# Performance work log

Measured on AMD Instinct MI355X. Metric: run time of the kernel, lower is better.

The kernel has to match this reference:

```python
import jax, jax.numpy as jnp
import numpy as np

B, S, HIDDEN = 2, 2048, 2048
HEADS, GROUPS, KVC = 16, 4, 128
HPG = HEADS // GROUPS  # heads per group
LAYER_INDEX = 2
SOFTMAX_SCALE = KVC ** -0.5
ROPE_THETA = 10000.0


def _rope_tables(seq_len, dim, dtype=jnp.float32):
    inv_freq = 1.0 / (ROPE_THETA ** (jnp.arange(0, dim, 2, dtype=jnp.float32) / dim))
    t = jnp.arange(seq_len, dtype=jnp.float32)
    freqs = jnp.outer(t, inv_freq)  # [S, dim/2]
    return jnp.cos(freqs).astype(dtype), jnp.sin(freqs).astype(dtype)


def _apply_rope(x, cos, sin):
    # x: [b, s, h, d]; rotate-half (GPT-NeoX style)
    d2 = x.shape[-1] // 2
    x1, x2 = x[..., :d2], x[..., d2:]
    c = cos[None, :, None, :]
    s = sin[None, :, None, :]
    return jnp.concatenate([x1 * c - x2 * s, x2 * c + x1 * s], axis=-1)


def setup_inputs() -> dict:
    key = jax.random.key(0)
    k1, k2, k3, k4 = jax.random.split(key, 4)
    std = HIDDEN ** -0.5
    return {
        "x": jax.random.normal(k1, (B, S, HIDDEN), dtype=jnp.float32),
        "w_q": jax.random.normal(k2, (HIDDEN, HEADS * KVC), dtype=jnp.float32) * std,
        "w_kv": jax.random.normal(k3, (HIDDEN, 2 * GROUPS * KVC), dtype=jnp.float32) * std,
        "w_dense": jax.random.normal(k4, (HEADS * KVC, HIDDEN), dtype=jnp.float32) * std,
    }


def reference(x, w_q, w_kv, w_dense):
    b, s, _ = x.shape
    # QKV projections
    q = (x @ w_q).reshape(b, s, HEADS, KVC)                 # [b,s,H,d]
    kv = (x @ w_kv).reshape(b, s, 2, GROUPS, KVC)
    k, v = kv[:, :, 0], kv[:, :, 1]                          # [b,s,G,d]
    # Rotary embeddings on q and k
    cos, sin = _rope_tables(s, KVC, x.dtype)
    q = _apply_rope(q, cos, sin)
    k = _apply_rope(k, cos, sin)
    # GQA attention with per-layer scaling trick:
    # scores computed at scale/softmax of layer_index, cast fp32, rescaled back.
    qg = q.reshape(b, s, GROUPS, HPG, KVC)
    scores = jnp.einsum("bqghd,bkgd->bghqk", qg, k) * (SOFTMAX_SCALE / LAYER_INDEX)
    scores = scores.astype(jnp.float32) * LAYER_INDEX
    # causal mask
    causal = jnp.tril(jnp.ones((s, s), dtype=bool))
    mask_value = jnp.finfo(jnp.float32).min
    scores = jnp.where(causal[None, None, None, :, :], scores, mask_value)
    probs = jax.nn.softmax(scores, axis=-1).astype(x.dtype)  # dropout p=0 (eval)
    ctx = jnp.einsum("bghqk,bkgd->bqghd", probs, v).reshape(b, s, HEADS * KVC)
    return ctx @ w_dense
```

## Files before the change

kernel.cpp:

```cpp
#include <hip/hip_runtime.h>
#include <hip/hip_bf16.h>
#include <stdint.h>

typedef unsigned short u16;
typedef __bf16 bf16x8 __attribute__((ext_vector_type(8)));
typedef float f32x4 __attribute__((ext_vector_type(4)));

#define S_LEN 2048
#define BATCH 2
#define NHEADS 16
#define NGROUPS 4
#define DHEAD 128
#define QKV_W 3072

__device__ __forceinline__ float bf2f(u16 u) {
  union { uint32_t i; float f; } v; v.i = ((uint32_t)u) << 16; return v.f;
}
__device__ __forceinline__ u16 f2bf(float f) {
  union { float f; uint32_t i; } v; v.f = f;
  uint32_t r = v.i + 0x7FFF + ((v.i >> 16) & 1);
  return (u16)(r >> 16);
}
__device__ __forceinline__ void llds16(const void* g, void* l) {
  __builtin_amdgcn_global_load_lds(
      (const __attribute__((address_space(1))) uint32_t*)g,
      (__attribute__((address_space(3))) uint32_t*)l, 16, 0, 0);
}

__device__ __forceinline__ void store_out(u16* C, long i, float v) { C[i] = f2bf(v); }
__device__ __forceinline__ void store_out(float* C, long i, float v) { C[i] = v; }

__global__ void rope_tables_k(float* __restrict__ cosT, float* __restrict__ sinT) {
  int i = blockIdx.x * 256 + threadIdx.x;
  int s = i >> 6, j = i & 63;
  float inv = exp2f(-(float)j * 0.20762050593045983f);
  float ang = (float)s * inv;
  float sv, cv;
  sincosf(ang, &sv, &cv);
  cosT[i] = cv; sinT[i] = sv;
}

__global__ void cvt_f32_bf16(const float* __restrict__ in, u16* __restrict__ out) {
  long i = ((long)blockIdx.x * 256 + threadIdx.x) * 4;
  float4 v = *(const float4*)(in + i);
  ushort4 o;
  o.x = f2bf(v.x); o.y = f2bf(v.y); o.z = f2bf(v.z); o.w = f2bf(v.w);
  *(ushort4*)(out + i) = o;
}

__global__ void transpose_f32_bf16(const float* __restrict__ in, u16* __restrict__ out,
                                   int R, int C) {
  __shared__ u16 tile[32][33];
  int c0 = blockIdx.x * 32, r0 = blockIdx.y * 32;
  int tx = threadIdx.x, ty = threadIdx.y;
  for (int i = 0; i < 32; i += 8)
    tile[ty + i][tx] = f2bf(in[(long)(r0 + ty + i) * C + c0 + tx]);
  __syncthreads();
  for (int i = 0; i < 32; i += 8)
    out[(long)(c0 + ty + i) * R + r0 + tx] = tile[tx][ty + i];
}

#define GFENCE() asm volatile("" ::: "memory")
#define MIDBAR() do { GFENCE(); __builtin_amdgcn_s_barrier(); \
    asm volatile("s_waitcnt lgkmcnt(0)" ::: "memory"); } while (0)
#define ENDBAR() do { GFENCE(); __builtin_amdgcn_s_barrier(); GFENCE(); } while (0)

__device__ __forceinline__ bf16x8 frag_ld(const __bf16* h, int wrow, int kk, int quad) {
  int b = ((wrow & 15) << 6) | (quad << 4);
  b ^= ((wrow >> 3) & 1) << 5;
  int off = ((((wrow >> 4) << 1) | kk) << 10) | b;
  return *(const bf16x8*)((const char*)h + off);
}

__device__ __forceinline__ void stage_half(const u16* __restrict__ g, int K,
                                           __bf16* lhalf, int wv, int lane) {
  int bsrc = (lane << 4) ^ (((lane >> 5) & 1) << 5);
  int r = bsrc >> 6, c = (bsrc & 63) >> 1;
  int cb = (wv & 1) << 5;
  llds16(g + (long)((wv >> 1) * 16 + r) * K + cb + c,
         lhalf + wv * 512 + lane * 8);
  llds16(g + (long)((4 + (wv >> 1)) * 16 + r) * K + cb + c,
         lhalf + 4096 + wv * 512 + lane * 8);
}

template <typename OutT>
__global__ __launch_bounds__(512) void gemm_bt8(
    const u16* __restrict__ A, const u16* __restrict__ Bt, OutT* __restrict__ C,
    int M, int N, int K) {
  __shared__ __align__(16) __bf16 lds[2][2][16384];
  const int tid = threadIdx.x;
  const int wv = tid >> 6, lane = tid & 63;
  const int quad = lane >> 4, l16 = lane & 15;
  const int wr = wv >> 2, wc = wv & 3;

  const int nwg = gridDim.x * gridDim.y;
  const int orig = blockIdx.y * gridDim.x + blockIdx.x;
  const int swz = (orig & 7) * (nwg >> 3) + (orig >> 3);
  const int bx = swz % gridDim.x, by = swz / gridDim.x;
  const int bm = by * 256, bn = bx * 256;

  const u16* Abase = A + (long)bm * K;
  const u16* Bbase = Bt + (long)bn * K;
  const int NT = K >> 6;

  f32x4 acc[8][4] = {};

  stage_half(Abase, K, &lds[0][0][0], wv, lane);
  stage_half(Abase + (long)128 * K, K, &lds[0][0][8192], wv, lane);
  stage_half(Bbase, K, &lds[0][1][0], wv, lane);
  stage_half(Bbase + (long)128 * K, K, &lds[0][1][8192], wv, lane);
  stage_half(Abase + 64, K, &lds[1][0][0], wv, lane);
  stage_half(Abase + (long)128 * K + 64, K, &lds[1][0][8192], wv, lane);
  stage_half(Bbase + 64, K, &lds[1][1][0], wv, lane);
  stage_half(Bbase + (long)128 * K + 64, K, &lds[1][1][8192], wv, lane);
  asm volatile("s_waitcnt vmcnt(8)" ::: "memory");
  __builtin_amdgcn_s_barrier();
  GFENCE();

  for (int kt = 0; kt < NT; ++kt) {
    const int buf = kt & 1;
    const __bf16* Ah = &lds[buf][0][wr * 8192];
    const __bf16* Bh = &lds[buf][1][(wc >> 1) * 8192];
    const int brow0 = (wc & 1) << 6;
    const bool pre = (kt + 2 < NT);
    bf16x8 aF[4][2], bF[4][2];

#pragma unroll
    for (int m = 0; m < 4; ++m) {
      aF[m][0] = frag_ld(Ah, m * 16 + l16, 0, quad);
      aF[m][1] = frag_ld(Ah, m * 16 + l16, 1, quad);
    }
#pragma unroll
    for (int n = 0; n < 2; ++n) {
      bF[n][0] = frag_ld(Bh, brow0 + n * 16 + l16, 0, quad);
      bF[n][1] = frag_ld(Bh, brow0 + n * 16 + l16, 1, quad);
    }
    MIDBAR();
    __builtin_amdgcn_s_setprio(1);
#pragma unroll
    for (int m = 0; m < 4; ++m)
#pragma unroll
      for (int n = 0; n < 2; ++n) {
        acc[m][n] = __builtin_amdgcn_mfma_f32_16x16x32_bf16(aF[m][0], bF[n][0], acc[m][n], 0, 0, 0);
        acc[m][n] = __builtin_amdgcn_mfma_f32_16x16x32_bf16(aF[m][1], bF[n][1], acc[m][n], 0, 0, 0);
      }
    __builtin_amdgcn_s_setprio(0);
    ENDBAR();

#pragma unroll
    for (int n = 2; n < 4; ++n) {
      bF[n][0] = frag_ld(Bh, brow0 + n * 16 + l16, 0, quad);
      bF[n][1] = frag_ld(Bh, brow0 + n * 16 + l16, 1, quad);
    }
    MIDBAR();
    __builtin_amdgcn_s_setprio(1);
#pragma unroll
    for (int m = 0; m < 4; ++m)
#pragma unroll
      for (int n = 2; n < 4; ++n) {
        acc[m][n] = __builtin_amdgcn_mfma_f32_16x16x32_bf16(aF[m][0], bF[n][0], acc[m][n], 0, 0, 0);
        acc[m][n] = __builtin_amdgcn_mfma_f32_16x16x32_bf16(aF[m][1], bF[n][1], acc[m][n], 0, 0, 0);
      }
    __builtin_amdgcn_s_setprio(0);
    ENDBAR();

#pragma unroll
    for (int m = 0; m < 4; ++m) {
      aF[m][0] = frag_ld(Ah, 64 + m * 16 + l16, 0, quad);
      aF[m][1] = frag_ld(Ah, 64 + m * 16 + l16, 1, quad);
    }
    if (pre) {
      const u16* p = Bbase + (long)(kt + 2) * 64;
      stage_half(p, K, &lds[buf][1][0], wv, lane);
      stage_half(p + (long)128 * K, K, &lds[buf][1][8192], wv, lane);
    }
    MIDBAR();
    __builtin_amdgcn_s_setprio(1);
#pragma unroll
    for (int m = 0; m < 4; ++m)
#pragma unroll
      for (int n = 2; n < 4; ++n) {
        acc[4 + m][n] = __builtin_amdgcn_mfma_f32_16x16x32_bf16(aF[m][0], bF[n][0], acc[4 + m][n], 0, 0, 0);
        acc[4 + m][n] = __builtin_amdgcn_mfma_f32_16x16x32_bf16(aF[m][1], bF[n][1], acc[4 + m][n], 0, 0, 0);
      }
    __builtin_amdgcn_s_setprio(0);
    ENDBAR();

    if (pre) {
      const u16* p = Abase + (long)(kt + 2) * 64;
      stage_half(p, K, &lds[buf][0][0], wv, lane);
      stage_half(p + (long)128 * K, K, &lds[buf][0][8192], wv, lane);
    }
    MIDBAR();
    __builtin_amdgcn_s_setprio(1);
#pragma unroll
    for (int m = 0; m < 4; ++m)
#pragma unroll
      for (int n = 0; n < 2; ++n) {
        acc[4 + m][n] = __builtin_amdgcn_mfma_f32_16x16x32_bf16(aF[m][0], bF[n][0], acc[4 + m][n], 0, 0, 0);
        acc[4 + m][n] = __builtin_amdgcn_mfma_f32_16x16x32_bf16(aF[m][1], bF[n][1], acc[4 + m][n], 0, 0, 0);
      }
    __builtin_amdgcn_s_setprio(0);
    if (pre) { asm volatile("s_waitcnt vmcnt(8)" ::: "memory"); }
    else     { asm volatile("s_waitcnt vmcnt(0)" ::: "memory"); }
    ENDBAR();
  }

  const long colbase = (long)bn + wc * 64 + l16;
#pragma unroll
  for (int mt = 0; mt < 8; ++mt)
#pragma unroll
    for (int nt = 0; nt < 4; ++nt)
#pragma unroll
      for (int rr = 0; rr < 4; ++rr) {
        long row = bm + wr * 128 + mt * 16 + quad * 4 + rr;
        store_out(C, row * N + colbase + nt * 16, acc[mt][nt][rr]);
      }
}

__global__ __launch_bounds__(512) void gemm_bt8n(
    const u16* __restrict__ A, const u16* __restrict__ Bt, float* __restrict__ C,
    int M, int N, int K) {
  __shared__ __align__(16) __bf16 Abuf[2][16384];
  __shared__ __align__(16) __bf16 Bbuf[2][8192];
  const int tid = threadIdx.x;
  const int wv = tid >> 6, lane = tid & 63;
  const int quad = lane >> 4, l16 = lane & 15;
  const int wr = wv >> 2, wc = wv & 3;

  const int nwg = gridDim.x * gridDim.y;
  const int orig = blockIdx.y * gridDim.x + blockIdx.x;
  const int swz = (orig & 7) * (nwg >> 3) + (orig >> 3);
  const int bx = swz % gridDim.x, by = swz / gridDim.x;
  const int bm = by * 256, bn = bx * 128;

  const u16* Abase = A + (long)bm * K;
  const u16* Bbase = Bt + (long)bn * K;
  const int NT = K >> 6;

  f32x4 acc[8][2] = {};

  stage_half(Abase, K, &Abuf[0][0], wv, lane);
  stage_half(Abase + (long)128 * K, K, &Abuf[0][8192], wv, lane);
  stage_half(Bbase, K, &Bbuf[0][0], wv, lane);
  stage_half(Abase + 64, K, &Abuf[1][0], wv, lane);
  stage_half(Abase + (long)128 * K + 64, K, &Abuf[1][8192], wv, lane);
  stage_half(Bbase + 64, K, &Bbuf[1][0], wv, lane);
  asm volatile("s_waitcnt vmcnt(0)" ::: "memory");
  __builtin_amdgcn_s_barrier();
  GFENCE();

  for (int kt = 0; kt < NT; ++kt) {
    const int buf = kt & 1;
    const __bf16* Ah = &Abuf[buf][wr * 8192];
    const __bf16* Bh = &Bbuf[buf][0];
    bf16x8 aF[4][2], bF[2][2];

#pragma unroll
    for (int m = 0; m < 4; ++m) {
      aF[m][0] = frag_ld(Ah, m * 16 + l16, 0, quad);
      aF[m][1] = frag_ld(Ah, m * 16 + l16, 1, quad);
    }
#pragma unroll
    for (int n = 0; n < 2; ++n) {
      bF[n][0] = frag_ld(Bh, wc * 32 + n * 16 + l16, 0, quad);
      bF[n][1] = frag_ld(Bh, wc * 32 + n * 16 + l16, 1, quad);
    }
    if (kt >= 1 && kt + 1 < NT) {
      const u16* p = Abase + (long)(kt + 1) * 64;
      stage_half(p, K, &Abuf[(kt + 1) & 1][0], wv, lane);
      stage_half(p + (long)128 * K, K, &Abuf[(kt + 1) & 1][8192], wv, lane);
    }
    MIDBAR();
    __builtin_amdgcn_s_setprio(1);
#pragma unroll
    for (int m = 0; m < 4; ++m)
#pragma unroll
      for (int n = 0; n < 2; ++n) {
        acc[m][n] = __builtin_amdgcn_mfma_f32_16x16x32_bf16(aF[m][0], bF[n][0], acc[m][n], 0, 0, 0);
        acc[m][n] = __builtin_amdgcn_mfma_f32_16x16x32_bf16(aF[m][1], bF[n][1], acc[m][n], 0, 0, 0);
      }
    __builtin_amdgcn_s_setprio(0);
    ENDBAR();

#pragma unroll
    for (int m = 0; m < 4; ++m) {
      aF[m][0] = frag_ld(Ah, 64 + m * 16 + l16, 0, quad);
      aF[m][1] = frag_ld(Ah, 64 + m * 16 + l16, 1, quad);
    }
    if (kt + 2 < NT) {
      stage_half(Bbase + (long)(kt + 2) * 64, K, &Bbuf[buf][0], wv, lane);
    }
    MIDBAR();
    __builtin_amdgcn_s_setprio(1);
#pragma unroll
    for (int m = 0; m < 4; ++m)
#pragma unroll
      for (int n = 0; n < 2; ++n) {
        acc[4 + m][n] = __builtin_amdgcn_mfma_f32_16x16x32_bf16(aF[m][0], bF[n][0], acc[4 + m][n], 0, 0, 0);
        acc[4 + m][n] = __builtin_amdgcn_mfma_f32_16x16x32_bf16(aF[m][1], bF[n][1], acc[4 + m][n], 0, 0, 0);
      }
    __builtin_amdgcn_s_setprio(0);
    if (kt + 2 < NT) { asm volatile("s_waitcnt vmcnt(2)" ::: "memory"); }
    else             { asm volatile("s_waitcnt vmcnt(0)" ::: "memory"); }
    ENDBAR();
  }

  const long colbase = (long)bn + wc * 32 + l16;
#pragma unroll
  for (int mt = 0; mt < 8; ++mt)
#pragma unroll
    for (int nt = 0; nt < 2; ++nt)
#pragma unroll
      for (int rr = 0; rr < 4; ++rr) {
        long row = bm + wr * 128 + mt * 16 + quad * 4 + rr;
        C[row * N + colbase + nt * 16] = acc[mt][nt][rr];
      }
}

__global__ void rope_k_k(const u16* __restrict__ qkv, u16* __restrict__ Kb,
                         const float* __restrict__ cosT, const float* __restrict__ sinT) {
  long i = (long)blockIdx.x * 256 + threadIdx.x;
  int j = i & 63;
  long rest = i >> 6;
  int g = rest & 3;
  long bs = rest >> 2;
  int s = bs & (S_LEN - 1);
  int b = (int)(bs >> 11);
  long src = bs * QKV_W + 2048 + g * 128 + j;
  float x1 = bf2f(qkv[src]), x2 = bf2f(qkv[src + 64]);
  float c = cosT[s * 64 + j], sn = sinT[s * 64 + j];
  long dst = ((long)(b * NGROUPS + g) * S_LEN + s) * DHEAD + j;
  Kb[dst] = f2bf(x1 * c - x2 * sn);
  Kb[dst + 64] = f2bf(x2 * c + x1 * sn);
}

__global__ void v_trans_k(const u16* __restrict__ qkv, u16* __restrict__ Vt) {
  __shared__ u16 tile[32][33];
  int s0 = blockIdx.x * 32, d0 = blockIdx.y * 32;
  int bg = blockIdx.z;
  int b = bg >> 2, g = bg & 3;
  int tx = threadIdx.x, ty = threadIdx.y;
  for (int i = 0; i < 32; i += 8) {
    long s = s0 + ty + i;
    tile[ty + i][tx] = qkv[((long)b * S_LEN + s) * QKV_W + 2560 + g * 128 + d0 + tx];
  }
  __syncthreads();
  for (int i = 0; i < 32; i += 8) {
    int d = d0 + ty + i;
    Vt[((long)(b * NGROUPS + g) * DHEAD + d) * S_LEN + s0 + tx] = tile[tx][ty + i];
  }
}

__global__ __launch_bounds__(512, 2) void attn_k10(
    const u16* __restrict__ Q,
    const u16* __restrict__ Kb,
    const u16* __restrict__ Vt,
    const float* __restrict__ cosT, const float* __restrict__ sinT,
    u16* __restrict__ ctx) {
  __shared__ __align__(16) char smem[82432];
  __bf16* Ks   = (__bf16*)smem;
  __bf16* Vts  = (__bf16*)(smem + 32768);
  __bf16* Ps   = (__bf16*)(smem + 65536);
  float*  Psum = (float*)(smem + 81920);
  float*  scr  = (float*)smem;

  const int h = blockIdx.y, b = blockIdx.z, g = h >> 2;
  const int tx = blockIdx.x;
  const int tid = threadIdx.x, wv = tid >> 6, lane = tid & 63;
  const int quad = lane >> 4, l16 = lane & 15;
  const int rg = wv & 3;
  const int kh = wv >> 2;
  const float SCALE = 0.08838834764831845f;

  const long kbase = (long)(b * NGROUPS + g) * S_LEN * DHEAD;
  const long vbase = (long)(b * NGROUPS + g) * DHEAD * S_LEN;

  const int krow_off = lane >> 4;
  const int vrow_off = lane >> 3;

  const __bf16 oneb = (__bf16)((l16 == 0) ? 1.0f : 0.0f);
  const bf16x8 bones = {oneb, oneb, oneb, oneb, oneb, oneb, oneb, oneb};

  __bf16* Pw = Ps + wv * 1024;

  for (int pass = 0; pass < 2; ++pass) {
    const int tile = pass ? (15 - tx) : tx;
    const int q0 = tile * 128;
    const int nch = 2 * (tile + 1);

    bf16x8 aq[2][4];
#pragma unroll
    for (int m = 0; m < 2; ++m) {
      const int srow = q0 + rg * 32 + m * 16 + l16;
      const u16* qp = Q + (long)(b * S_LEN + srow) * QKV_W + h * DHEAD + quad * 8;
      bf16x8 raw[4];
#pragma unroll
      for (int ds = 0; ds < 4; ++ds)
        raw[ds] = *(const bf16x8*)(qp + ds * 32);
      const float* cb = cosT + srow * 64 + quad * 8;
      const float* sb = sinT + srow * 64 + quad * 8;
#pragma unroll
      for (int ds = 0; ds < 2; ++ds)
#pragma unroll
        for (int e = 0; e < 8; ++e) {
          float c = cb[ds * 32 + e], s = sb[ds * 32 + e];
          float lo = (float)raw[ds][e], hi = (float)raw[ds + 2][e];
          aq[m][ds][e]     = (__bf16)(lo * c - hi * s);
          aq[m][ds + 2][e] = (__bf16)(hi * c + lo * s);
        }
    }

#pragma unroll
    for (int i = 0; i < 2; ++i) {
      int r0 = wv * 8 + i * 4;
      int row = r0 + krow_off;
      int c = l16 ^ (row & 15);
      llds16(Kb + kbase + (long)row * DHEAD + c * 8, &Ks[r0 * 128 + lane * 8]);
    }
#pragma unroll
    for (int i = 0; i < 2; ++i) {
      int d0 = wv * 16 + i * 8;
      int row = d0 + vrow_off;
      int c = (lane & 7) ^ (row & 7);
      llds16(Vt + vbase + (long)row * S_LEN + c * 8, &Vts[d0 * 64 + lane * 8]);
    }
    __syncthreads();

    f32x4 Oacc[2][8] = {};
    f32x4 Osum[2] = {};
    const int rmin = q0 + rg * 32;

    for (int kc = 0; kc < nch; ++kc) {
      const int cur = kc & 1;
      if (kc + 1 < nch) {
        const int nxt = cur ^ 1;
#pragma unroll
        for (int i = 0; i < 2; ++i) {
          int r0 = wv * 8 + i * 4;
          int row = r0 + krow_off;
          int c = l16 ^ (row & 15);
          llds16(Kb + kbase + (long)((kc + 1) * 64 + row) * DHEAD + c * 8,
                 &Ks[nxt * 8192 + r0 * 128 + lane * 8]);
        }
#pragma unroll
        for (int i = 0; i < 2; ++i) {
          int d0 = wv * 16 + i * 8;
          int row = d0 + vrow_off;
          int c = (lane & 7) ^ (row & 7);
          llds16(Vt + vbase + (long)row * S_LEN + (kc + 1) * 64 + c * 8,
                 &Vts[nxt * 8192 + d0 * 64 + lane * 8]);
        }
      }

      const int kb0 = kc * 64 + kh * 32;
      const bool skip = kb0 > (rmin + 31);
      if (!skip) {
        f32x4 sacc[2][2] = {};
        __builtin_amdgcn_s_setprio(1);
#pragma unroll
        for (int ds = 0; ds < 4; ++ds) {
          int pos0 = ((ds * 4 + quad) ^ l16) * 8;
#pragma unroll
          for (int nt = 0; nt < 2; ++nt) {
            bf16x8 bk = *(const bf16x8*)&Ks[cur * 8192 + (kh * 32 + nt * 16 + l16) * 128 + pos0];
            sacc[0][nt] = __builtin_amdgcn_mfma_f32_16x16x32_bf16(aq[0][ds], bk, sacc[0][nt], 0, 0, 0);
            sacc[1][nt] = __builtin_amdgcn_mfma_f32_16x16x32_bf16(aq[1][ds], bk, sacc[1][nt], 0, 0, 0);
          }
        }
        __builtin_amdgcn_s_setprio(0);

        const bool need_mask = (kb0 + 31) > rmin;
        if (need_mask) {
#pragma unroll
          for (int m = 0; m < 2; ++m)
#pragma unroll
            for (int nt = 0; nt < 2; ++nt)
#pragma unroll
              for (int r = 0; r < 4; ++r) {
                int qrow = rmin + m * 16 + quad * 4 + r;
                int key = kb0 + nt * 16 + l16;
                float p = (key <= qrow) ? __expf(sacc[m][nt][r] * SCALE) : 0.f;
                int row = m * 16 + quad * 4 + r;
                int gs = (nt * 2 + (l16 >> 3)) ^ quad;
                Pw[row * 32 + gs * 8 + (l16 & 7)] = (__bf16)p;
              }
        } else {
#pragma unroll
          for (int m = 0; m < 2; ++m)
#pragma unroll
            for (int nt = 0; nt < 2; ++nt)
#pragma unroll
              for (int r = 0; r < 4; ++r) {
                float p = __expf(sacc[m][nt][r] * SCALE);
                int row = m * 16 + quad * 4 + r;
                int gs = (nt * 2 + (l16 >> 3)) ^ quad;
                Pw[row * 32 + gs * 8 + (l16 & 7)] = (__bf16)p;
              }
        }

        bf16x8 ap[2];
#pragma unroll
        for (int m = 0; m < 2; ++m) {
          int pos = (quad ^ ((l16 >> 2) & 3)) * 8;
          ap[m] = *(const bf16x8*)&Pw[(m * 16 + l16) * 32 + pos];
        }
        __builtin_amdgcn_s_setprio(1);
#pragma unroll
        for (int nt = 0; nt < 8; ++nt) {
          int pos = (((kh << 2) | quad) ^ (l16 & 7)) * 8;
          bf16x8 bv = *(const bf16x8*)&Vts[cur * 8192 + (nt * 16 + l16) * 64 + pos];
          Oacc[0][nt] = __builtin_amdgcn_mfma_f32_16x16x32_bf16(ap[0], bv, Oacc[0][nt], 0, 0, 0);
          Oacc[1][nt] = __builtin_amdgcn_mfma_f32_16x16x32_bf16(ap[1], bv, Oacc[1][nt], 0, 0, 0);
        }
#pragma unroll
        for (int m = 0; m < 2; ++m)
          Osum[m] = __builtin_amdgcn_mfma_f32_16x16x32_bf16(ap[m], bones, Osum[m], 0, 0, 0);
        __builtin_amdgcn_s_setprio(0);
      }

      __syncthreads();
    }

    if (kh == 1) {
      float* s = scr + rg * 4096;
#pragma unroll
      for (int m = 0; m < 2; ++m)
#pragma unroll
        for (int nt = 0; nt < 8; ++nt)
#pragma unroll
          for (int r = 0; r < 4; ++r)
            s[(m * 16 + quad * 4 + r) * 128 + nt * 16 + l16] = Oacc[m][nt][r];
      if (l16 == 0) {
#pragma unroll
        for (int m = 0; m < 2; ++m)
#pragma unroll
          for (int r = 0; r < 4; ++r)
            Psum[rg * 32 + m * 16 + quad * 4 + r] = Osum[m][r];
      }
    }
    __syncthreads();
    if (kh == 0) {
      float* s = scr + rg * 4096;
#pragma unroll
      for (int m = 0; m < 2; ++m) {
        float lsum[4];
#pragma unroll
        for (int r = 0; r < 4; ++r)
          lsum[r] = __shfl(Osum[m][r], quad << 4, 64) +
                    Psum[rg * 32 + m * 16 + quad * 4 + r];
        const long obase = ((long)(b * S_LEN + q0 + rg * 32 + m * 16) * NHEADS + h) * DHEAD;
#pragma unroll
        for (int nt = 0; nt < 8; ++nt)
#pragma unroll
          for (int r = 0; r < 4; ++r) {
            int lrow = quad * 4 + r;
            float v = Oacc[m][nt][r] + s[(m * 16 + lrow) * 128 + nt * 16 + l16];
            ctx[obase + (long)lrow * NHEADS * DHEAD + nt * 16 + l16] = f2bf(v / lsum[r]);
          }
      }
    }
    __syncthreads();
  }
}

extern "C" void kernel_launch(void* const* d_in, const int* in_sizes, int n_in,
                              void* d_out, int out_size, void* d_ws, size_t ws_size,
                              hipStream_t stream) {
  const float* x   = (const float*)d_in[0];
  const float* wq  = (const float*)d_in[1];
  const float* wkv = (const float*)d_in[2];
  const float* wd  = (const float*)d_in[3];
  float* out = (float*)d_out;

  char* ws = (char*)d_ws;
  float* cosT  = (float*)(ws + 0);
  float* sinT  = (float*)(ws + 524288);
  u16* wqkvT = (u16*)(ws + 1048576);
  u16* wdT   = (u16*)(ws + 13631488);
  u16* xb    = (u16*)(ws + 22020096);
  u16* qkv   = (u16*)(ws + 38797312);
  u16* Kb    = (u16*)(ws + 63963136);
  u16* Vt    = (u16*)(ws + 68157440);
  u16* ctx   = (u16*)(ws + 72351744);

  rope_tables_k<<<512, 256, 0, stream>>>(cosT, sinT);
  cvt_f32_bf16<<<8192, 256, 0, stream>>>(x, xb);
  transpose_f32_bf16<<<dim3(64, 64), dim3(32, 8), 0, stream>>>(wq, wqkvT, 2048, 2048);
  transpose_f32_bf16<<<dim3(32, 64), dim3(32, 8), 0, stream>>>(wkv, wqkvT + (long)2048 * 2048, 2048, 1024);
  transpose_f32_bf16<<<dim3(64, 64), dim3(32, 8), 0, stream>>>(wd, wdT, 2048, 2048);

  gemm_bt8<u16><<<dim3(12, 16), 512, 0, stream>>>(xb, wqkvT, qkv, 4096, 3072, 2048);

  rope_k_k<<<4096, 256, 0, stream>>>(qkv, Kb, cosT, sinT);
  v_trans_k<<<dim3(64, 4, 8), dim3(32, 8), 0, stream>>>(qkv, Vt);

  attn_k10<<<dim3(8, 16, 2), 512, 0, stream>>>(qkv, Kb, Vt, cosT, sinT, ctx);

  gemm_bt8n<<<dim3(16, 16), 512, 0, stream>>>(ctx, wdT, out, 4096, 2048, 2048);
}
```

Baseline: 290.9 us.

## Use 256x192 QKV GEMM tiles and share P buffer per row group in attention

The QKV projection GEMM now uses 256x192 output tiles, giving a 16x16 grid of 256 workgroups instead of 12x16. This is meant to fill all compute units on the MI355X (256 CUs) and avoid a partially occupied wave. The attention kernel now stages its P tile in a buffer shared by each row group, with a 64-wide XOR swizzle, instead of one buffer per wave. That change alters LDS bank patterns and may need the two key-half waves to agree on the layout. Smaller N tiles lower the arithmetic intensity per tile and cost more B traffic per FLOP.

Measured after the change: 284.9 us. 2.1% less time.

```diff
diff --git a/kernel.cpp b/kernel.cpp
--- a/kernel.cpp
+++ b/kernel.cpp
@@ -26,9 +26,6 @@
       (const __attribute__((address_space(1))) uint32_t*)g,
       (__attribute__((address_space(3))) uint32_t*)l, 16, 0, 0);
 }
-
-__device__ __forceinline__ void store_out(u16* C, long i, float v) { C[i] = f2bf(v); }
-__device__ __forceinline__ void store_out(float* C, long i, float v) { C[i] = v; }
 
 __global__ void rope_tables_k(float* __restrict__ cosT, float* __restrict__ sinT) {
   int i = blockIdx.x * 256 + threadIdx.x;
@@ -72,22 +69,24 @@
   return *(const bf16x8*)((const char*)h + off);
 }
 
-__device__ __forceinline__ void stage_half(const u16* __restrict__ g, int K,
-                                           __bf16* lhalf, int wv, int lane) {
+__device__ __forceinline__ void stage_u64(const u16* __restrict__ g, int K,
+                                          __bf16* ldsu, int wv, int lane) {
   int bsrc = (lane << 4) ^ (((lane >> 5) & 1) << 5);
   int r = bsrc >> 6, c = (bsrc & 63) >> 1;
   int cb = (wv & 1) << 5;
-  llds16(g + (long)((wv >> 1) * 16 + r) * K + cb + c,
-         lhalf + wv * 512 + lane * 8);
-  llds16(g + (long)((4 + (wv >> 1)) * 16 + r) * K + cb + c,
-         lhalf + 4096 + wv * 512 + lane * 8);
-}
-
-template <typename OutT>
-__global__ __launch_bounds__(512) void gemm_bt8(
-    const u16* __restrict__ A, const u16* __restrict__ Bt, OutT* __restrict__ C,
+  llds16(g + (long)((wv >> 1) * 16 + r) * K + cb + c, ldsu + wv * 512 + lane * 8);
+}
+__device__ __forceinline__ void stage_half(const u16* __restrict__ g, int K,
+                                           __bf16* lhalf, int wv, int lane) {
+  stage_u64(g, K, lhalf, wv, lane);
+  stage_u64(g + (long)64 * K, K, lhalf + 4096, wv, lane);
+}
+
+__global__ __launch_bounds__(512) void gemm_btw(
+    const u16* __restrict__ A, const u16* __restrict__ Bt, u16* __restrict__ C,
     int M, int N, int K) {
-  __shared__ __align__(16) __bf16 lds[2][2][16384];
+  __shared__ __align__(16) __bf16 Abuf[2][16384];
+  __shared__ __align__(16) __bf16 Bbuf[2][12288];
   const int tid = threadIdx.x;
   const int wv = tid >> 6, lane = tid & 63;
   const int quad = lane >> 4, l16 = lane & 15;
@@ -97,67 +96,63 @@
   const int orig = blockIdx.y * gridDim.x + blockIdx.x;
   const int swz = (orig & 7) * (nwg >> 3) + (orig >> 3);
   const int bx = swz % gridDim.x, by = swz / gridDim.x;
-  const int bm = by * 256, bn = bx * 256;
+  const int bm = by * 256, bn = bx * 192;
 
   const u16* Abase = A + (long)bm * K;
   const u16* Bbase = Bt + (long)bn * K;
   const int NT = K >> 6;
 
-  f32x4 acc[8][4] = {};
-
-  stage_half(Abase, K, &lds[0][0][0], wv, lane);
-  stage_half(Abase + (long)128 * K, K, &lds[0][0][8192], wv, lane);
-  stage_half(Bbase, K, &lds[0][1][0], wv, lane);
-  stage_half(Bbase + (long)128 * K, K, &lds[0][1][8192], wv, lane);
-  stage_half(Abase + 64, K, &lds[1][0][0], wv, lane);
-  stage_half(Abase + (long)128 * K + 64, K, &lds[1][0][8192], wv, lane);
-  stage_half(Bbase + 64, K, &lds[1][1][0], wv, lane);
-  stage_half(Bbase + (long)128 * K + 64, K, &lds[1][1][8192], wv, lane);
-  asm volatile("s_waitcnt vmcnt(8)" ::: "memory");
+  f32x4 acc[8][3] = {};
+
+#pragma unroll
+  for (int t = 0; t < 2; ++t) {
+#pragma unroll
+    for (int u = 0; u < 4; ++u)
+      stage_u64(Abase + (long)u * 64 * K + t * 64, K, &Abuf[t][u * 4096], wv, lane);
+#pragma unroll
+    for (int u = 0; u < 3; ++u)
+      stage_u64(Bbase + (long)u * 64 * K + t * 64, K, &Bbuf[t][u * 4096], wv, lane);
+  }
+  asm volatile("s_waitcnt vmcnt(7)" ::: "memory");
   __builtin_amdgcn_s_barrier();
   GFENCE();
 
   for (int kt = 0; kt < NT; ++kt) {
     const int buf = kt & 1;
-    const __bf16* Ah = &lds[buf][0][wr * 8192];
-    const __bf16* Bh = &lds[buf][1][(wc >> 1) * 8192];
-    const int brow0 = (wc & 1) << 6;
+    const __bf16* Ah = &Abuf[buf][wr * 8192];
+    const __bf16* Bh = &Bbuf[buf][0];
+    const int bn0 = wc * 48;
     const bool pre = (kt + 2 < NT);
-    bf16x8 aF[4][2], bF[4][2];
+    bf16x8 aF[4][2], bF[3][2];
 
 #pragma unroll
     for (int m = 0; m < 4; ++m) {
       aF[m][0] = frag_ld(Ah, m * 16 + l16, 0, quad);
       aF[m][1] = frag_ld(Ah, m * 16 + l16, 1, quad);
     }
-#pragma unroll
-    for (int n = 0; n < 2; ++n) {
-      bF[n][0] = frag_ld(Bh, brow0 + n * 16 + l16, 0, quad);
-      bF[n][1] = frag_ld(Bh, brow0 + n * 16 + l16, 1, quad);
-    }
+    bF[0][0] = frag_ld(Bh, bn0 + l16, 0, quad);
+    bF[0][1] = frag_ld(Bh, bn0 + l16, 1, quad);
     MIDBAR();
     __builtin_amdgcn_s_setprio(1);
 #pragma unroll
-    for (int m = 0; m < 4; ++m)
-#pragma unroll
-      for (int n = 0; n < 2; ++n) {
-        acc[m][n] = __builtin_amdgcn_mfma_f32_16x16x32_bf16(aF[m][0], bF[n][0], acc[m][n], 0, 0, 0);
-        acc[m][n] = __builtin_amdgcn_mfma_f32_16x16x32_bf16(aF[m][1], bF[n][1], acc[m][n], 0, 0, 0);
-      }
+    for (int m = 0; m < 4; ++m) {
+      acc[m][0] = __builtin_amdgcn_mfma_f32_16x16x32_bf16(aF[m][0], bF[0][0], acc[m][0], 0, 0, 0);
+      acc[m][0] = __builtin_amdgcn_mfma_f32_16x16x32_bf16(aF[m][1], bF[0][1], acc[m][0], 0, 0, 0);
+    }
     __builtin_amdgcn_s_setprio(0);
     ENDBAR();
 
 #pragma unroll
-    for (int n = 2; n < 4; ++n) {
-      bF[n][0] = frag_ld(Bh, brow0 + n * 16 + l16, 0, quad);
-      bF[n][1] = frag_ld(Bh, brow0 + n * 16 + l16, 1, quad);
+    for (int n = 1; n < 3; ++n) {
+      bF[n][0] = frag_ld(Bh, bn0 + n * 16 + l16, 0, quad);
+      bF[n][1] = frag_ld(Bh, bn0 + n * 16 + l16, 1, quad);
     }
     MIDBAR();
     __builtin_amdgcn_s_setprio(1);
 #pragma unroll
     for (int m = 0; m < 4; ++m)
 #pragma unroll
-      for (int n = 2; n < 4; ++n) {
+      for (int n = 1; n < 3; ++n) {
         acc[m][n] = __builtin_amdgcn_mfma_f32_16x16x32_bf16(aF[m][0], bF[n][0], acc[m][n], 0, 0, 0);
         acc[m][n] = __builtin_amdgcn_mfma_f32_16x16x32_bf16(aF[m][1], bF[n][1], acc[m][n], 0, 0, 0);
       }
@@ -170,16 +165,17 @@
       aF[m][1] = frag_ld(Ah, 64 + m * 16 + l16, 1, quad);
     }
     if (pre) {
-      const u16* p = Bbase + (long)(kt + 2) * 64;
-      stage_half(p, K, &lds[buf][1][0], wv, lane);
-      stage_half(p + (long)128 * K, K, &lds[buf][1][8192], wv, lane);
+#pragma unroll
+      for (int u = 0; u < 3; ++u)
+        stage_u64(Bbase + (long)u * 64 * K + (long)(kt + 2) * 64, K,
+                  &Bbuf[buf][u * 4096], wv, lane);
     }
     MIDBAR();
     __builtin_amdgcn_s_setprio(1);
 #pragma unroll
     for (int m = 0; m < 4; ++m)
 #pragma unroll
-      for (int n = 2; n < 4; ++n) {
+      for (int n = 1; n < 3; ++n) {
         acc[4 + m][n] = __builtin_amdgcn_mfma_f32_16x16x32_bf16(aF[m][0], bF[n][0], acc[4 + m][n], 0, 0, 0);
         acc[4 + m][n] = __builtin_amdgcn_mfma_f32_16x16x32_bf16(aF[m][1], bF[n][1], acc[4 + m][n], 0, 0, 0);
       }
@@ -187,34 +183,33 @@
     ENDBAR();
 
     if (pre) {
-      const u16* p = Abase + (long)(kt + 2) * 64;
-      stage_half(p, K, &lds[buf][0][0], wv, lane);
-      stage_half(p + (long)128 * K, K, &lds[buf][0][8192], wv, lane);
+#pragma unroll
+      for (int u = 0; u < 4; ++u)
+        stage_u64(Abase + (long)u * 64 * K + (long)(kt + 2) * 64, K,
+                  &Abuf[buf][u * 4096], wv, lane);
     }
     MIDBAR();
     __builtin_amdgcn_s_setprio(1);
 #pragma unroll
-    for (int m = 0; m < 4; ++m)
-#pragma unroll
-      for (int n = 0; n < 2; ++n) {
-        acc[4 + m][n] = __builtin_amdgcn_mfma_f32_16x16x32_bf16(aF[m][0], bF[n][0], acc[4 + m][n], 0, 0, 0);
-        acc[4 + m][n] = __builtin_amdgcn_mfma_f32_16x16x32_bf16(aF[m][1], bF[n][1], acc[4 + m][n], 0, 0, 0);
-      }
+    for (int m = 0; m < 4; ++m) {
+      acc[4 + m][0] = __builtin_amdgcn_mfma_f32_16x16x32_bf16(aF[m][0], bF[0][0], acc[4 + m][0], 0, 0, 0);
+      acc[4 + m][0] = __builtin_amdgcn_mfma_f32_16x16x32_bf16(aF[m][1], bF[0][1], acc[4 + m][0], 0, 0, 0);
+    }
     __builtin_amdgcn_s_setprio(0);
-    if (pre) { asm volatile("s_waitcnt vmcnt(8)" ::: "memory"); }
+    if (pre) { asm volatile("s_waitcnt vmcnt(7)" ::: "memory"); }
     else     { asm volatile("s_waitcnt vmcnt(0)" ::: "memory"); }
     ENDBAR();
   }
 
-  const long colbase = (long)bn + wc * 64 + l16;
+  const long colbase = (long)bn + wc * 48 + l16;
 #pragma unroll
   for (int mt = 0; mt < 8; ++mt)
 #pragma unroll
-    for (int nt = 0; nt < 4; ++nt)
+    for (int nt = 0; nt < 3; ++nt)
 #pragma unroll
       for (int rr = 0; rr < 4; ++rr) {
         long row = bm + wr * 128 + mt * 16 + quad * 4 + rr;
-        store_out(C, row * N + colbase + nt * 16, acc[mt][nt][rr]);
+        C[row * N + colbase + nt * 16] = f2bf(acc[mt][nt][rr]);
       }
 }
 
@@ -352,7 +347,7 @@
   }
 }
 
-__global__ __launch_bounds__(512, 2) void attn_k10(
+__global__ __launch_bounds__(512, 2) void attn_k11(
     const u16* __restrict__ Q,
     const u16* __restrict__ Kb,
     const u16* __restrict__ Vt,
@@ -382,7 +377,7 @@
   const __bf16 oneb = (__bf16)((l16 == 0) ? 1.0f : 0.0f);
   const bf16x8 bones = {oneb, oneb, oneb, oneb, oneb, oneb, oneb, oneb};
 
-  __bf16* Pw = Ps + wv * 1024;
+  __bf16* Prg = Ps + rg * 2048;
 
   for (int pass = 0; pass < 2; ++pass) {
     const int tile = pass ? (15 - tx) : tx;
@@ -482,8 +477,9 @@
                 int key = kb0 + nt * 16 + l16;
                 float p = (key <= qrow) ? __expf(sacc[m][nt][r] * SCALE) : 0.f;
                 int row = m * 16 + quad * 4 + r;
-                int gs = (nt * 2 + (l16 >> 3)) ^ quad;
-                Pw[row * 32 + gs * 8 + (l16 & 7)] = (__bf16)p;
+                int gq = kh * 4 + nt * 2 + (l16 >> 3);
+                int pos = gq ^ (row & 7);
+                Prg[row * 64 + pos * 8 + (l16 & 7)] = (__bf16)p;
               }
         } else {
 #pragma unroll
@@ -494,16 +490,17 @@
               for (int r = 0; r < 4; ++r) {
                 float p = __expf(sacc[m][nt][r] * SCALE);
                 int row = m * 16 + quad * 4 + r;
-                int gs = (nt * 2 + (l16 >> 3)) ^ quad;
-                Pw[row * 32 + gs * 8 + (l16 & 7)] = (__bf16)p;
+                int gq = kh * 4 + nt * 2 + (l16 >> 3);
+                int pos = gq ^ (row & 7);
+                Prg[row * 64 + pos * 8 + (l16 & 7)] = (__bf16)p;
               }
         }
 
         bf16x8 ap[2];
 #pragma unroll
         for (int m = 0; m < 2; ++m) {
-          int pos = (quad ^ ((l16 >> 2) & 3)) * 8;
-          ap[m] = *(const bf16x8*)&Pw[(m * 16 + l16) * 32 + pos];
+          int pos = (kh * 4 + quad) ^ (l16 & 7);
+          ap[m] = *(const bf16x8*)&Prg[(m * 16 + l16) * 64 + pos * 8];
         }
         __builtin_amdgcn_s_setprio(1);
 #pragma unroll
@@ -590,12 +587,12 @@
   transpose_f32_bf16<<<dim3(32, 64), dim3(32, 8), 0, stream>>>(wkv, wqkvT + (long)2048 * 2048, 2048, 1024);
   transpose_f32_bf16<<<dim3(64, 64), dim3(32, 8), 0, stream>>>(wd, wdT, 2048, 2048);
 
-  gemm_bt8<u16><<<dim3(12, 16), 512, 0, stream>>>(xb, wqkvT, qkv, 4096, 3072, 2048);
+  gemm_btw<<<dim3(16, 16), 512, 0, stream>>>(xb, wqkvT, qkv, 4096, 3072, 2048);
 
   rope_k_k<<<4096, 256, 0, stream>>>(qkv, Kb, cosT, sinT);
   v_trans_k<<<dim3(64, 4, 8), dim3(32, 8), 0, stream>>>(qkv, Vt);
 
-  attn_k10<<<dim3(8, 16, 2), 512, 0, stream>>>(qkv, Kb, Vt, cosT, sinT, ctx);
+  attn_k11<<<dim3(8, 16, 2), 512, 0, stream>>>(qkv, Kb, Vt, cosT, sinT, ctx);
 
   gemm_bt8n<<<dim3(16, 16), 512, 0, stream>>>(ctx, wdT, out, 4096, 2048, 2048);
 }
```
